# Optimization experiments

Hardware: AMD Instinct MI355X
Metric: run time of the kernel (lower is better)

## Reference

```python
import jax, jax.numpy as jnp
import numpy as np

N = 100000   # nodes
E = 1600000  # edges
IN, HID, OUT = 128, 128, 64

def setup_inputs() -> dict:
    key = jax.random.key(0)
    ks = jax.random.split(key, 18)
    def lin(k, i, o):
        kw, kb = jax.random.split(k)
        s = 1.0 / np.sqrt(i)
        return (jax.random.uniform(kw, (i, o), jnp.float32, -s, s),
                jax.random.uniform(kb, (o,), jnp.float32, -s, s))
    x = jax.random.normal(ks[0], (N, IN), jnp.float32)
    edge_index = jax.random.randint(ks[1], (2, E), 0, N, jnp.int64)
    W1, b1   = lin(ks[2], IN, HID)
    W21, b21 = lin(ks[3], IN, HID)
    W22, b22 = lin(ks[4], HID, HID)
    W31, b31 = lin(ks[5], IN, HID)
    W32, b32 = lin(ks[6], HID, HID)
    W33, b33 = lin(ks[7], HID, HID)
    Wa, ba   = lin(ks[8], HID, 1)
    Wf, bf   = lin(ks[9], HID, OUT)
    return dict(x=x, edge_index=edge_index, W1=W1, b1=b1, W21=W21, b21=b21,
                W22=W22, b22=b22, W31=W31, b31=b31, W32=W32, b32=b32,
                W33=W33, b33=b33, Wa=Wa, ba=ba, Wf=Wf, bf=bf)

def _gcn(x, W, b, src, dst, dinv):
    # PyG GCNConv: D^{-1/2}(A+I)D^{-1/2} X W + b, self-loops added.
    h = x @ W                                    # [N, F]
    norm = dinv[src] * dinv[dst]                 # [E]
    agg = jax.ops.segment_sum(h[src] * norm[:, None], dst, num_segments=N)
    agg = agg + h * (dinv * dinv)[:, None]       # self-loop contribution
    return agg + b

def reference(x, edge_index, W1, b1, W21, b21, W22, b22, W31, b31,
              W32, b32, W33, b33, Wa, ba, Wf, bf):
    src, dst = edge_index[0], edge_index[1]
    # degree with self-loops (in-degree at target nodes)
    deg = jax.ops.segment_sum(jnp.ones(E, x.dtype), dst, num_segments=N) + 1.0
    dinv = jax.lax.rsqrt(deg)
    h1 = jax.nn.relu(_gcn(x, W1, b1, src, dst, dinv))
    h2 = jax.nn.relu(_gcn(x, W21, b21, src, dst, dinv))
    h2 = jax.nn.relu(_gcn(h2, W22, b22, src, dst, dinv))
    h3 = jax.nn.relu(_gcn(x, W31, b31, src, dst, dinv))
    h3 = jax.nn.relu(_gcn(h3, W32, b32, src, dst, dinv))
    h3 = jax.nn.relu(_gcn(h3, W33, b33, src, dst, dinv))
    H = jnp.stack([h1, h2, h3], axis=1)          # [N, 3, HID]
    scores = H @ Wa + ba                         # [N, 3, 1]
    w = jax.nn.softmax(scores, axis=1)
    h_meta = jnp.sum(w * H, axis=1)              # [N, HID]
    h_out = h_meta + h1
    return h_out @ Wf + bf                       # [N, OUT]
```

## Files before the change

### kernel.cpp

```cpp
#include <hip/hip_runtime.h>
#include <hip/hip_bf16.h>

#define HIDF 128
#define OUTF 64
#define SCAN_B 256
#define BK_SHIFT 7

typedef __attribute__((ext_vector_type(8))) short bf16x8;
typedef __attribute__((ext_vector_type(4))) float f32x4;

__device__ __forceinline__ float us2f(unsigned u_lo16) {
    return __uint_as_float(u_lo16 << 16);
}
__device__ __forceinline__ unsigned short f2us(float f) {
    __hip_bfloat16 h = __float2bfloat16(f);
    return *reinterpret_cast<unsigned short*>(&h);
}
__device__ __forceinline__ unsigned pack2(float a, float b) {
    return (unsigned)f2us(a) | ((unsigned)f2us(b) << 16);
}

__global__ __launch_bounds__(256) void deg_zero(int* __restrict__ d, int N) {
    int i = blockIdx.x * 256 + threadIdx.x;
    if (i < N) d[i] = 0;
}

__global__ __launch_bounds__(256) void deg_count(const int* __restrict__ ei, int* __restrict__ d, int E) {
    int e = blockIdx.x * 256 + threadIdx.x;
    if (e < E) atomicAdd(&d[ei[E + e]], 1);
}

__global__ __launch_bounds__(256) void scanA(const int* __restrict__ degi, int* __restrict__ blocksum, int N) {
    __shared__ int red[256];
    const int b = blockIdx.x;
    const int chunk = (N + SCAN_B - 1) / SCAN_B;
    const int lo = b * chunk, hi = min(lo + chunk, N);
    int s = 0;
    for (int i = lo + threadIdx.x; i < hi; i += 256) s += degi[i];
    red[threadIdx.x] = s;
    __syncthreads();
    for (int off = 128; off; off >>= 1) {
        if (threadIdx.x < off) red[threadIdx.x] += red[threadIdx.x + off];
        __syncthreads();
    }
    if (threadIdx.x == 0) blocksum[b] = red[0];
}

__global__ __launch_bounds__(256) void scanB(const int* __restrict__ blocksum, int* __restrict__ blockoff) {
    __shared__ int ps[256];
    const int t = threadIdx.x;
    ps[t] = blocksum[t];
    __syncthreads();
    for (int off = 1; off < 256; off <<= 1) {
        int v = ps[t];
        int u = (t >= off) ? ps[t - off] : 0;
        __syncthreads();
        ps[t] = v + u;
        __syncthreads();
    }
    blockoff[t] = (t == 0) ? 0 : ps[t - 1];
}

__global__ __launch_bounds__(256) void scanC(const int* __restrict__ degi,
                                             const int* __restrict__ blockoff,
                                             int* __restrict__ cursor,
                                             float* __restrict__ dinv, int N) {
    __shared__ int ps[256];
    const int b = blockIdx.x;
    const int chunk = (N + SCAN_B - 1) / SCAN_B;
    const int lo = b * chunk, hi = min(lo + chunk, N);
    const int tchunk = (chunk + 255) / 256;
    const int tlo = lo + threadIdx.x * tchunk;
    const int thi = min(tlo + tchunk, hi);
    int s = 0;
    for (int i = tlo; i < thi; ++i) s += degi[i];
    ps[threadIdx.x] = s;
    __syncthreads();
    for (int off = 1; off < 256; off <<= 1) {
        int v = ps[threadIdx.x];
        int u = (threadIdx.x >= off) ? ps[threadIdx.x - off] : 0;
        __syncthreads();
        ps[threadIdx.x] = v + u;
        __syncthreads();
    }
    int base = blockoff[b] + ((threadIdx.x == 0) ? 0 : ps[threadIdx.x - 1]);
    for (int i = tlo; i < thi; ++i) {
        int d = degi[i];
        cursor[i] = base;
        base += d;
        dinv[i] = rsqrtf((float)d + 1.f);
    }
}

__global__ __launch_bounds__(256) void bcur_init(const int* __restrict__ cursor,
                                                 int* __restrict__ bcur, int N, int NBK) {
    int b = blockIdx.x * 256 + threadIdx.x;
    if (b < NBK) bcur[b * 64] = cursor[b << BK_SHIFT];
}

__global__ __launch_bounds__(256) void bucket_scatter(const int* __restrict__ ei,
                                                      int* __restrict__ bcur,
                                                      int2* __restrict__ edg, int E) {
    int e = blockIdx.x * 256 + threadIdx.x;
    if (e >= E) return;
    int src = ei[e];
    int dst = ei[E + e];
    int pos = atomicAdd(&bcur[(dst >> BK_SHIFT) * 64], 1);
    edg[pos] = make_int2(src, dst);
}

__global__ __launch_bounds__(256) void final_scatter(const int2* __restrict__ edg,
                                                     int* __restrict__ cursor,
                                                     int* __restrict__ csr_src, int E) {
    int p = blockIdx.x * 256 + threadIdx.x;
    if (p >= E) return;
    int2 sd = edg[p];
    int pos = atomicAdd(&cursor[sd.y], 1);
    csr_src[pos] = sd.x;
}

__global__ __launch_bounds__(256) void cvt_scale(const float* __restrict__ X,
                                                 const float* __restrict__ dinv,
                                                 unsigned short* __restrict__ TB, int N) {
    int g = blockIdx.x * 256 + threadIdx.x;
    if (g >= N * 32) return;
    int n = g >> 5;
    float dv = dinv[n];
    float4 v = ((const float4*)X)[g];
    ushort4 o;
    o.x = f2us(v.x * dv); o.y = f2us(v.y * dv);
    o.z = f2us(v.z * dv); o.w = f2us(v.w * dv);
    ((ushort4*)TB)[g] = o;
}

__global__ __launch_bounds__(256) void cvt_w(const float* __restrict__ Wa0,
                                             const float* __restrict__ Wa1,
                                             const float* __restrict__ Wa2,
                                             const float* __restrict__ Wa3,
                                             const float* __restrict__ Wa4,
                                             const float* __restrict__ Wa5,
                                             unsigned short* __restrict__ WTB) {
    int t = blockIdx.x * 256 + threadIdx.x;
    if (t >= 6 * 16384) return;
    int m = t >> 14, local = t & 16383;
    int n = local >> 7, k = local & 127;
    const float* src = (m == 0) ? Wa0 : (m == 1) ? Wa1 : (m == 2) ? Wa2
                     : (m == 3) ? Wa3 : (m == 4) ? Wa4 : Wa5;
    WTB[t] = f2us(src[k * 128 + n]);
}

template <bool OUT_BF16>
__global__ __launch_bounds__(256) void agg_b(const unsigned short* __restrict__ TB,
                                             const float* __restrict__ dinv,
                                             const int* __restrict__ csr_src,
                                             const int* __restrict__ rend,
                                             void* __restrict__ O, int N) {
    const int n = (blockIdx.x * 256 + threadIdx.x) >> 6;
    const int lane = threadIdx.x & 63;
    if (n >= N) return;
    const int start = (n == 0) ? 0 : rend[n - 1];
    const int end   = rend[n];
    const unsigned* Tv = (const unsigned*)TB;

    float ax0 = 0.f, ay0 = 0.f, ax1 = 0.f, ay1 = 0.f;
    int e = start;
    for (; e + 8 <= end; e += 8) {
        int s0 = csr_src[e + 0], s1 = csr_src[e + 1], s2 = csr_src[e + 2], s3 = csr_src[e + 3];
        int s4 = csr_src[e + 4], s5 = csr_src[e + 5], s6 = csr_src[e + 6], s7 = csr_src[e + 7];
        unsigned v0 = Tv[(size_t)s0 * 64 + lane];
        unsigned v1 = Tv[(size_t)s1 * 64 + lane];
        unsigned v2 = Tv[(size_t)s2 * 64 + lane];
        unsigned v3 = Tv[(size_t)s3 * 64 + lane];
        unsigned v4 = Tv[(size_t)s4 * 64 + lane];
        unsigned v5 = Tv[(size_t)s5 * 64 + lane];
        unsigned v6 = Tv[(size_t)s6 * 64 + lane];
        unsigned v7 = Tv[(size_t)s7 * 64 + lane];
        ax0 += us2f(v0 & 0xffffu); ay0 += __uint_as_float(v0 & 0xffff0000u);
        ax1 += us2f(v1 & 0xffffu); ay1 += __uint_as_float(v1 & 0xffff0000u);
        ax0 += us2f(v2 & 0xffffu); ay0 += __uint_as_float(v2 & 0xffff0000u);
        ax1 += us2f(v3 & 0xffffu); ay1 += __uint_as_float(v3 & 0xffff0000u);
        ax0 += us2f(v4 & 0xffffu); ay0 += __uint_as_float(v4 & 0xffff0000u);
        ax1 += us2f(v5 & 0xffffu); ay1 += __uint_as_float(v5 & 0xffff0000u);
        ax0 += us2f(v6 & 0xffffu); ay0 += __uint_as_float(v6 & 0xffff0000u);
        ax1 += us2f(v7 & 0xffffu); ay1 += __uint_as_float(v7 & 0xffff0000u);
    }
    if (e + 4 <= end) {
        int s0 = csr_src[e + 0], s1 = csr_src[e + 1], s2 = csr_src[e + 2], s3 = csr_src[e + 3];
        unsigned v0 = Tv[(size_t)s0 * 64 + lane];
        unsigned v1 = Tv[(size_t)s1 * 64 + lane];
        unsigned v2 = Tv[(size_t)s2 * 64 + lane];
        unsigned v3 = Tv[(size_t)s3 * 64 + lane];
        ax0 += us2f(v0 & 0xffffu); ay0 += __uint_as_float(v0 & 0xffff0000u);
        ax1 += us2f(v1 & 0xffffu); ay1 += __uint_as_float(v1 & 0xffff0000u);
        ax0 += us2f(v2 & 0xffffu); ay0 += __uint_as_float(v2 & 0xffff0000u);
        ax1 += us2f(v3 & 0xffffu); ay1 += __uint_as_float(v3 & 0xffff0000u);
        e += 4;
    }
    for (; e < end; ++e) {
        int s = csr_src[e];
        unsigned v = Tv[(size_t)s * 64 + lane];
        ax0 += us2f(v & 0xffffu);
        ay0 += __uint_as_float(v & 0xffff0000u);
    }
    unsigned sv = Tv[(size_t)n * 64 + lane];
    ax0 += us2f(sv & 0xffffu);
    ay0 += __uint_as_float(sv & 0xffff0000u);
    const float dv = dinv[n];
    float ox = (ax0 + ax1) * dv;
    float oy = (ay0 + ay1) * dv;
    if (OUT_BF16) {
        ((unsigned*)O)[(size_t)n * 64 + lane] = pack2(ox, oy);
    } else {
        float2 o; o.x = ox; o.y = oy;
        ((float2*)O)[(size_t)n * 64 + lane] = o;
    }
}

__global__ __launch_bounds__(256) void agg_dual(const unsigned short* __restrict__ TB23,
                                                const float* __restrict__ dinv,
                                                const int* __restrict__ csr_src,
                                                const int* __restrict__ rend,
                                                unsigned* __restrict__ OA,
                                                unsigned* __restrict__ OB, int N) {
    const int n = (blockIdx.x * 256 + threadIdx.x) >> 6;
    const int lane = threadIdx.x & 63;
    if (n >= N) return;
    const int start = (n == 0) ? 0 : rend[n - 1];
    const int end   = rend[n];
    const unsigned* Tv = (const unsigned*)TB23;

    float ax2 = 0.f, ay2 = 0.f, bx2 = 0.f, by2 = 0.f;
    float ax3 = 0.f, ay3 = 0.f, bx3 = 0.f, by3 = 0.f;
    int e = start;
    for (; e + 4 <= end; e += 4) {
        int s0 = csr_src[e + 0], s1 = csr_src[e + 1], s2 = csr_src[e + 2], s3 = csr_src[e + 3];
        unsigned a0 = Tv[(size_t)s0 * 128 + lane];
        unsigned c0 = Tv[(size_t)s0 * 128 + 64 + lane];
        unsigned a1 = Tv[(size_t)s1 * 128 + lane];
        unsigned c1 = Tv[(size_t)s1 * 128 + 64 + lane];
        unsigned a2 = Tv[(size_t)s2 * 128 + lane];
        unsigned c2 = Tv[(size_t)s2 * 128 + 64 + lane];
        unsigned a3 = Tv[(size_t)s3 * 128 + lane];
        unsigned c3 = Tv[(size_t)s3 * 128 + 64 + lane];
        ax2 += us2f(a0 & 0xffffu); ay2 += __uint_as_float(a0 & 0xffff0000u);
        ax3 += us2f(c0 & 0xffffu); ay3 += __uint_as_float(c0 & 0xffff0000u);
        bx2 += us2f(a1 & 0xffffu); by2 += __uint_as_float(a1 & 0xffff0000u);
        bx3 += us2f(c1 & 0xffffu); by3 += __uint_as_float(c1 & 0xffff0000u);
        ax2 += us2f(a2 & 0xffffu); ay2 += __uint_as_float(a2 & 0xffff0000u);
        ax3 += us2f(c2 & 0xffffu); ay3 += __uint_as_float(c2 & 0xffff0000u);
        bx2 += us2f(a3 & 0xffffu); by2 += __uint_as_float(a3 & 0xffff0000u);
        bx3 += us2f(c3 & 0xffffu); by3 += __uint_as_float(c3 & 0xffff0000u);
    }
    for (; e < end; ++e) {
        int s = csr_src[e];
        unsigned a = Tv[(size_t)s * 128 + lane];
        unsigned c = Tv[(size_t)s * 128 + 64 + lane];
        ax2 += us2f(a & 0xffffu); ay2 += __uint_as_float(a & 0xffff0000u);
        ax3 += us2f(c & 0xffffu); ay3 += __uint_as_float(c & 0xffff0000u);
    }
    {
        unsigned a = Tv[(size_t)n * 128 + lane];
        unsigned c = Tv[(size_t)n * 128 + 64 + lane];
        ax2 += us2f(a & 0xffffu); ay2 += __uint_as_float(a & 0xffff0000u);
        ax3 += us2f(c & 0xffffu); ay3 += __uint_as_float(c & 0xffff0000u);
    }
    const float dv = dinv[n];
    OA[(size_t)n * 64 + lane] = pack2((ax2 + bx2) * dv, (ay2 + by2) * dv);
    OB[(size_t)n * 64 + lane] = pack2((ax3 + bx3) * dv, (ay3 + by3) * dv);
}

#define OM_F32 0
#define OM_BF16 1
#define OM_BF16_SR 2
template <int OMODE, int OSTRIDE>
__global__ __launch_bounds__(256) void gemm_mfma(const unsigned short* __restrict__ Xb,
                                                 const unsigned short* __restrict__ WT,
                                                 const float* __restrict__ bias,
                                                 const float* __restrict__ dinv,
                                                 void* __restrict__ T, int N) {
    __shared__ unsigned short Xs[64 * 128];
    __shared__ unsigned short Ws[128 * 128];
    const int tid = threadIdx.x;
    const int nb = blockIdx.x * 64;

    for (int c = tid; c < 2048; c += 256) {
        int n = c >> 4, kc = c & 15;
        ((uint4*)Ws)[(n << 4) | (kc ^ (n & 7))] = ((const uint4*)WT)[c];
    }
    for (int c = tid; c < 1024; c += 256) {
        int nl = c >> 4, kc = c & 15;
        int n = nb + nl;
        uint4 v = make_uint4(0u, 0u, 0u, 0u);
        if (n < N) v = ((const uint4*)(Xb + (size_t)n * HIDF))[kc];
        ((uint4*)Xs)[(nl << 4) | (kc ^ (nl & 7))] = v;
    }
    __syncthreads();

    const int wv   = tid >> 6;
    const int l    = tid & 63;
    const int row  = l & 15;
    const int kgrp = l >> 4;

    bf16x8 afr[4];
    #pragma unroll
    for (int kk = 0; kk < 4; ++kk) {
        int nl = 16 * wv + row;
        int kc = kk * 4 + kgrp;
        afr[kk] = *(const bf16x8*)(Xs + nl * 128 + ((kc ^ (nl & 7)) << 3));
    }

    f32x4 acc[8];
    #pragma unroll
    for (int nt = 0; nt < 8; ++nt) {
        float b = bias[nt * 16 + row];
        acc[nt] = (f32x4){b, b, b, b};
    }

    #pragma unroll
    for (int nt = 0; nt < 8; ++nt) {
        int col = nt * 16 + row;
        #pragma unroll
        for (int kk = 0; kk < 4; ++kk) {
            int kc = kk * 4 + kgrp;
            bf16x8 bfr = *(const bf16x8*)(Ws + col * 128 + ((kc ^ (col & 7)) << 3));
            acc[nt] = __builtin_amdgcn_mfma_f32_16x16x32_bf16(afr[kk], bfr, acc[nt], 0, 0, 0);
        }
    }

    float dv[4];
    if (OMODE == OM_BF16_SR) {
        #pragma unroll
        for (int r = 0; r < 4; ++r) {
            int grow = nb + 16 * wv + kgrp * 4 + r;
            dv[r] = (grow < N) ? dinv[grow] : 0.f;
        }
    }
    #pragma unroll
    for (int nt = 0; nt < 8; ++nt) {
        int gcol = nt * 16 + row;
        #pragma unroll
        for (int r = 0; r < 4; ++r) {
            int grow = nb + 16 * wv + kgrp * 4 + r;
            if (grow < N) {
                float v = acc[nt][r];
                if (OMODE == OM_BF16_SR) v = fmaxf(v, 0.f) * dv[r];
                if (OMODE == OM_F32) {
                    ((float*)T)[(size_t)grow * OSTRIDE + gcol] = v;
                } else {
                    ((unsigned short*)T)[(size_t)grow * OSTRIDE + gcol] = f2us(v);
                }
            }
        }
    }
}

__global__ __launch_bounds__(256) void meta_kernel(const float* __restrict__ H1,
                                                   const unsigned short* __restrict__ H2B,
                                                   const unsigned short* __restrict__ H3B,
                                                   const float* __restrict__ Wa,
                                                   const float* __restrict__ ba,
                                                   const float* __restrict__ Wf,
                                                   const float* __restrict__ bfb,
                                                   float* __restrict__ out, int N) {
    __shared__ float WfS[HIDF * OUTF];
    __shared__ float WaS[HIDF];
    __shared__ float hm[4][HIDF];
    const int tid = threadIdx.x;
    for (int i = tid; i < HIDF * OUTF; i += 256) WfS[i] = Wf[i];
    if (tid < HIDF) WaS[tid] = Wa[tid];
    __syncthreads();
    const float bav = ba[0];
    const int w = tid >> 6;
    const int l = tid & 63;
    const float bfv = bfb[l];
    const int iters = (N + 3) >> 2;

    for (int it = blockIdx.x; it < iters; it += gridDim.x) {
        const int n = it * 4 + w;
        __syncthreads();
        if (n < N) {
            const float* h1 = H1 + (size_t)n * HIDF;
            const unsigned short* h2 = H2B + (size_t)n * HIDF;
            const unsigned short* h3 = H3B + (size_t)n * HIDF;
            float h1a = fmaxf(h1[l], 0.f),       h1b = fmaxf(h1[l + 64], 0.f);
            float h2a = fmaxf(us2f(h2[l]), 0.f), h2b = fmaxf(us2f(h2[l + 64]), 0.f);
            float h3a = fmaxf(us2f(h3[l]), 0.f), h3b = fmaxf(us2f(h3[l + 64]), 0.f);
            float s1 = h1a * WaS[l] + h1b * WaS[l + 64];
            float s2 = h2a * WaS[l] + h2b * WaS[l + 64];
            float s3 = h3a * WaS[l] + h3b * WaS[l + 64];
            #pragma unroll
            for (int off = 32; off; off >>= 1) {
                s1 += __shfl_xor(s1, off);
                s2 += __shfl_xor(s2, off);
                s3 += __shfl_xor(s3, off);
            }
            s1 += bav; s2 += bav; s3 += bav;
            float m  = fmaxf(s1, fmaxf(s2, s3));
            float e1 = expf(s1 - m), e2 = expf(s2 - m), e3 = expf(s3 - m);
            float inv = 1.f / (e1 + e2 + e3);
            float w1 = e1 * inv, w2 = e2 * inv, w3 = e3 * inv;
            hm[w][l]      = w1 * h1a + w2 * h2a + w3 * h3a + h1a;
            hm[w][l + 64] = w1 * h1b + w2 * h2b + w3 * h3b + h1b;
        }
        __syncthreads();
        if (n < N) {
            float acc = bfv;
            #pragma unroll
            for (int k = 0; k < HIDF; ++k) acc = fmaf(hm[w][k], WfS[k * OUTF + l], acc);
            out[(size_t)n * OUTF + l] = acc;
        }
    }
}

extern "C" void kernel_launch(void* const* d_in, const int* in_sizes, int n_in,
                              void* d_out, int out_size, void* d_ws, size_t ws_size,
                              hipStream_t stream) {
    const float* x   = (const float*)d_in[0];
    const int*   ei  = (const int*)d_in[1];
    const float *W1  = (const float*)d_in[2],  *b1  = (const float*)d_in[3];
    const float *W21 = (const float*)d_in[4],  *b21 = (const float*)d_in[5];
    const float *W22 = (const float*)d_in[6],  *b22 = (const float*)d_in[7];
    const float *W31 = (const float*)d_in[8],  *b31 = (const float*)d_in[9];
    const float *W32 = (const float*)d_in[10], *b32 = (const float*)d_in[11];
    const float *W33 = (const float*)d_in[12], *b33 = (const float*)d_in[13];
    const float *Wa  = (const float*)d_in[14], *ba  = (const float*)d_in[15];
    const float *Wf  = (const float*)d_in[16], *bfb = (const float*)d_in[17];

    const int N = in_sizes[0] / HIDF;
    const int E = in_sizes[1] / 2;
    const int NBK = (N + 127) >> BK_SHIFT;

    int*   DEGI    = (int*)d_ws;
    int*   CURSOR  = DEGI + N;
    int*   CSR_SRC = CURSOR + N;
    int2*  EDG     = (int2*)(CSR_SRC + E);
    int*   BCUR    = (int*)(EDG + E);
    int*   BSUM    = BCUR + 1024 * 64;
    int*   BOFF    = BSUM + 256;
    float* DINV    = (float*)(BOFF + 256);
    unsigned short* TB23 = (unsigned short*)(DINV + N);
    unsigned* PXB  = (unsigned*)(TB23 + (size_t)N * 256);
    unsigned* AGA  = PXB + (size_t)N * 64;
    unsigned* AGB  = AGA + (size_t)N * 64;
    unsigned* H2B  = AGB + (size_t)N * 64;
    unsigned short* WTB = (unsigned short*)(H2B + (size_t)N * 64);

    const int gN    = (N + 255) / 256;
    const int gE    = (E + 255) / 256;
    const int gCVT  = (N * 32 + 255) / 256;
    const int gAGG  = (N * 64 + 255) / 256;
    const int gGEMM = (N + 63) / 64;
    const int gMETA = 2048;

    deg_zero<<<gN, 256, 0, stream>>>(DEGI, N);
    deg_count<<<gE, 256, 0, stream>>>(ei, DEGI, E);
    scanA<<<SCAN_B, 256, 0, stream>>>(DEGI, BSUM, N);
    scanB<<<1, 256, 0, stream>>>(BSUM, BOFF);
    scanC<<<SCAN_B, 256, 0, stream>>>(DEGI, BOFF, CURSOR, DINV, N);
    bcur_init<<<(NBK + 255) / 256, 256, 0, stream>>>(CURSOR, BCUR, N, NBK);
    bucket_scatter<<<gE, 256, 0, stream>>>(ei, BCUR, EDG, E);
    final_scatter<<<gE, 256, 0, stream>>>(EDG, CURSOR, CSR_SRC, E);
    cvt_w<<<384, 256, 0, stream>>>(W21, W31, W22, W32, W33, W1, WTB);

    unsigned short* TBX = TB23;

    cvt_scale<<<gCVT, 256, 0, stream>>>(x, DINV, TBX, N);
    agg_b<true><<<gAGG, 256, 0, stream>>>(TBX, DINV, CSR_SRC, CURSOR, PXB, N);

    gemm_mfma<OM_BF16_SR, 256><<<gGEMM, 256, 0, stream>>>((unsigned short*)PXB, WTB,         b21, DINV, TB23,       N);
    gemm_mfma<OM_BF16_SR, 256><<<gGEMM, 256, 0, stream>>>((unsigned short*)PXB, WTB + 16384, b31, DINV, TB23 + 128, N);
    agg_dual<<<gAGG, 256, 0, stream>>>(TB23, DINV, CSR_SRC, CURSOR, AGA, AGB, N);

    gemm_mfma<OM_BF16, 128><<<gGEMM, 256, 0, stream>>>((unsigned short*)AGA, WTB + 2 * 16384, b22, DINV, H2B, N);
    gemm_mfma<OM_BF16_SR, 128><<<gGEMM, 256, 0, stream>>>((unsigned short*)AGB, WTB + 3 * 16384, b32, DINV, TBX, N);
    agg_b<true><<<gAGG, 256, 0, stream>>>(TBX, DINV, CSR_SRC, CURSOR, AGA, N);
    gemm_mfma<OM_BF16, 128><<<gGEMM, 256, 0, stream>>>((unsigned short*)AGA, WTB + 4 * 16384, b33, DINV, AGB, N);

    float* H1F = (float*)TB23;
    gemm_mfma<OM_F32, 128><<<gGEMM, 256, 0, stream>>>((unsigned short*)PXB, WTB + 5 * 16384, b1, DINV, H1F, N);

    meta_kernel<<<gMETA, 256, 0, stream>>>(H1F, (const unsigned short*)H2B,
                                           (const unsigned short*)AGB, Wa, ba, Wf, bfb,
                                           (float*)d_out, N);
}
```

Baseline: 726.6 us.

## Pack bucketed edges, per-bucket final scatter, wider gathers in aggregation kernels

Bucketed edges are now packed into one 32-bit word (source shifted, with the low destination bits), halving the intermediate edge buffer. The final scatter runs one block per 128-node bucket instead of one thread per edge. The aggregation kernels gather 8-byte uint2 chunks: a wave covers two edges at once with half-waves, reduced by a shuffle, and the dual kernel reads both feature sets per lane contiguously. The meta kernel reads packed pairs. Edge packing assumes source ids fit in 25 bits, and the wider loads change the summation order.

```diff
diff --git a/kernel.cpp b/kernel.cpp
--- a/kernel.cpp
+++ b/kernel.cpp
@@ -11,6 +11,9 @@
 
 __device__ __forceinline__ float us2f(unsigned u_lo16) {
     return __uint_as_float(u_lo16 << 16);
+}
+__device__ __forceinline__ float hi2f(unsigned u) {
+    return __uint_as_float(u & 0xffff0000u);
 }
 __device__ __forceinline__ unsigned short f2us(float f) {
     __hip_bfloat16 h = __float2bfloat16(f);
@@ -100,23 +103,33 @@
 
 __global__ __launch_bounds__(256) void bucket_scatter(const int* __restrict__ ei,
                                                       int* __restrict__ bcur,
-                                                      int2* __restrict__ edg, int E) {
+                                                      unsigned* __restrict__ edg, int E) {
     int e = blockIdx.x * 256 + threadIdx.x;
     if (e >= E) return;
     int src = ei[e];
     int dst = ei[E + e];
     int pos = atomicAdd(&bcur[(dst >> BK_SHIFT) * 64], 1);
-    edg[pos] = make_int2(src, dst);
-}
-
-__global__ __launch_bounds__(256) void final_scatter(const int2* __restrict__ edg,
-                                                     int* __restrict__ cursor,
-                                                     int* __restrict__ csr_src, int E) {
-    int p = blockIdx.x * 256 + threadIdx.x;
-    if (p >= E) return;
-    int2 sd = edg[p];
-    int pos = atomicAdd(&cursor[sd.y], 1);
-    csr_src[pos] = sd.x;
+    edg[pos] = ((unsigned)src << BK_SHIFT) | (unsigned)(dst & ((1 << BK_SHIFT) - 1));
+}
+
+__global__ __launch_bounds__(256) void final_scatter_b(const unsigned* __restrict__ edg,
+                                                       const int* __restrict__ bcur,
+                                                       int* __restrict__ cursor,
+                                                       int* __restrict__ csr_src) {
+    const int b = blockIdx.x;
+    __shared__ int sstart;
+    if (threadIdx.x == 0) sstart = cursor[b << BK_SHIFT];
+    __syncthreads();
+    const int bstart = sstart;
+    const int bend   = bcur[b * 64];
+    const int base   = b << BK_SHIFT;
+    for (int p = bstart + threadIdx.x; p < bend; p += 256) {
+        unsigned u = edg[p];
+        int src = (int)(u >> BK_SHIFT);
+        int dst = base | (int)(u & ((1u << BK_SHIFT) - 1));
+        int pos = atomicAdd(&cursor[dst], 1);
+        csr_src[pos] = src;
+    }
 }
 
 __global__ __launch_bounds__(256) void cvt_scale(const float* __restrict__ X,
@@ -149,124 +162,102 @@
     WTB[t] = f2us(src[k * 128 + n]);
 }
 
-template <bool OUT_BF16>
-__global__ __launch_bounds__(256) void agg_b(const unsigned short* __restrict__ TB,
-                                             const float* __restrict__ dinv,
-                                             const int* __restrict__ csr_src,
-                                             const int* __restrict__ rend,
-                                             void* __restrict__ O, int N) {
+__global__ __launch_bounds__(256) void agg_b2(const unsigned short* __restrict__ TB,
+                                              const float* __restrict__ dinv,
+                                              const int* __restrict__ csr_src,
+                                              const int* __restrict__ rend,
+                                              unsigned* __restrict__ O, int N) {
     const int n = (blockIdx.x * 256 + threadIdx.x) >> 6;
-    const int lane = threadIdx.x & 63;
+    const int l = threadIdx.x & 63;
+    if (n >= N) return;
+    const int half = l >> 5;
+    const int sl   = l & 31;
+    const int start = (n == 0) ? 0 : rend[n - 1];
+    const int end   = rend[n];
+    const uint2* Tv = (const uint2*)TB;
+
+    float a0 = 0.f, a1 = 0.f, a2 = 0.f, a3 = 0.f;
+    int e = start;
+    for (; e + 8 <= end; e += 8) {
+        int sA = csr_src[e + 0 + half];
+        int sB = csr_src[e + 2 + half];
+        int sC = csr_src[e + 4 + half];
+        int sD = csr_src[e + 6 + half];
+        uint2 vA = Tv[(size_t)sA * 32 + sl];
+        uint2 vB = Tv[(size_t)sB * 32 + sl];
+        uint2 vC = Tv[(size_t)sC * 32 + sl];
+        uint2 vD = Tv[(size_t)sD * 32 + sl];
+        a0 += us2f(vA.x & 0xffffu); a1 += hi2f(vA.x); a2 += us2f(vA.y & 0xffffu); a3 += hi2f(vA.y);
+        a0 += us2f(vB.x & 0xffffu); a1 += hi2f(vB.x); a2 += us2f(vB.y & 0xffffu); a3 += hi2f(vB.y);
+        a0 += us2f(vC.x & 0xffffu); a1 += hi2f(vC.x); a2 += us2f(vC.y & 0xffffu); a3 += hi2f(vC.y);
+        a0 += us2f(vD.x & 0xffffu); a1 += hi2f(vD.x); a2 += us2f(vD.y & 0xffffu); a3 += hi2f(vD.y);
+    }
+    for (; e + 2 <= end; e += 2) {
+        int s = csr_src[e + half];
+        uint2 v = Tv[(size_t)s * 32 + sl];
+        a0 += us2f(v.x & 0xffffu); a1 += hi2f(v.x); a2 += us2f(v.y & 0xffffu); a3 += hi2f(v.y);
+    }
+    if (e < end && half == 0) {
+        int s = csr_src[e];
+        uint2 v = Tv[(size_t)s * 32 + sl];
+        a0 += us2f(v.x & 0xffffu); a1 += hi2f(v.x); a2 += us2f(v.y & 0xffffu); a3 += hi2f(v.y);
+    }
+    if (half == 0) {
+        uint2 v = Tv[(size_t)n * 32 + sl];
+        a0 += us2f(v.x & 0xffffu); a1 += hi2f(v.x); a2 += us2f(v.y & 0xffffu); a3 += hi2f(v.y);
+    }
+    a0 += __shfl_xor(a0, 32); a1 += __shfl_xor(a1, 32);
+    a2 += __shfl_xor(a2, 32); a3 += __shfl_xor(a3, 32);
+    if (half == 0) {
+        const float dv = dinv[n];
+        uint2 o;
+        o.x = pack2(a0 * dv, a1 * dv);
+        o.y = pack2(a2 * dv, a3 * dv);
+        ((uint2*)O)[(size_t)n * 32 + sl] = o;
+    }
+}
+
+__global__ __launch_bounds__(256) void agg_dual2(const unsigned short* __restrict__ TB23,
+                                                 const float* __restrict__ dinv,
+                                                 const int* __restrict__ csr_src,
+                                                 const int* __restrict__ rend,
+                                                 unsigned* __restrict__ OA,
+                                                 unsigned* __restrict__ OB, int N) {
+    const int n = (blockIdx.x * 256 + threadIdx.x) >> 6;
+    const int l = threadIdx.x & 63;
     if (n >= N) return;
     const int start = (n == 0) ? 0 : rend[n - 1];
     const int end   = rend[n];
-    const unsigned* Tv = (const unsigned*)TB;
-
-    float ax0 = 0.f, ay0 = 0.f, ax1 = 0.f, ay1 = 0.f;
-    int e = start;
-    for (; e + 8 <= end; e += 8) {
-        int s0 = csr_src[e + 0], s1 = csr_src[e + 1], s2 = csr_src[e + 2], s3 = csr_src[e + 3];
-        int s4 = csr_src[e + 4], s5 = csr_src[e + 5], s6 = csr_src[e + 6], s7 = csr_src[e + 7];
-        unsigned v0 = Tv[(size_t)s0 * 64 + lane];
-        unsigned v1 = Tv[(size_t)s1 * 64 + lane];
-        unsigned v2 = Tv[(size_t)s2 * 64 + lane];
-        unsigned v3 = Tv[(size_t)s3 * 64 + lane];
-        unsigned v4 = Tv[(size_t)s4 * 64 + lane];
-        unsigned v5 = Tv[(size_t)s5 * 64 + lane];
-        unsigned v6 = Tv[(size_t)s6 * 64 + lane];
-        unsigned v7 = Tv[(size_t)s7 * 64 + lane];
-        ax0 += us2f(v0 & 0xffffu); ay0 += __uint_as_float(v0 & 0xffff0000u);
-        ax1 += us2f(v1 & 0xffffu); ay1 += __uint_as_float(v1 & 0xffff0000u);
-        ax0 += us2f(v2 & 0xffffu); ay0 += __uint_as_float(v2 & 0xffff0000u);
-        ax1 += us2f(v3 & 0xffffu); ay1 += __uint_as_float(v3 & 0xffff0000u);
-        ax0 += us2f(v4 & 0xffffu); ay0 += __uint_as_float(v4 & 0xffff0000u);
-        ax1 += us2f(v5 & 0xffffu); ay1 += __uint_as_float(v5 & 0xffff0000u);
-        ax0 += us2f(v6 & 0xffffu); ay0 += __uint_as_float(v6 & 0xffff0000u);
-        ax1 += us2f(v7 & 0xffffu); ay1 += __uint_as_float(v7 & 0xffff0000u);
-    }
-    if (e + 4 <= end) {
-        int s0 = csr_src[e + 0], s1 = csr_src[e + 1], s2 = csr_src[e + 2], s3 = csr_src[e + 3];
-        unsigned v0 = Tv[(size_t)s0 * 64 + lane];
-        unsigned v1 = Tv[(size_t)s1 * 64 + lane];
-        unsigned v2 = Tv[(size_t)s2 * 64 + lane];
-        unsigned v3 = Tv[(size_t)s3 * 64 + lane];
-        ax0 += us2f(v0 & 0xffffu); ay0 += __uint_as_float(v0 & 0xffff0000u);
-        ax1 += us2f(v1 & 0xffffu); ay1 += __uint_as_float(v1 & 0xffff0000u);
-        ax0 += us2f(v2 & 0xffffu); ay0 += __uint_as_float(v2 & 0xffff0000u);
-        ax1 += us2f(v3 & 0xffffu); ay1 += __uint_as_float(v3 & 0xffff0000u);
-        e += 4;
-    }
-    for (; e < end; ++e) {
-        int s = csr_src[e];
-        unsigned v = Tv[(size_t)s * 64 + lane];
-        ax0 += us2f(v & 0xffffu);
-        ay0 += __uint_as_float(v & 0xffff0000u);
-    }
-    unsigned sv = Tv[(size_t)n * 64 + lane];
-    ax0 += us2f(sv & 0xffffu);
-    ay0 += __uint_as_float(sv & 0xffff0000u);
-    const float dv = dinv[n];
-    float ox = (ax0 + ax1) * dv;
-    float oy = (ay0 + ay1) * dv;
-    if (OUT_BF16) {
-        ((unsigned*)O)[(size_t)n * 64 + lane] = pack2(ox, oy);
-    } else {
-        float2 o; o.x = ox; o.y = oy;
-        ((float2*)O)[(size_t)n * 64 + lane] = o;
-    }
-}
-
-__global__ __launch_bounds__(256) void agg_dual(const unsigned short* __restrict__ TB23,
-                                                const float* __restrict__ dinv,
-                                                const int* __restrict__ csr_src,
-                                                const int* __restrict__ rend,
-                                                unsigned* __restrict__ OA,
-                                                unsigned* __restrict__ OB, int N) {
-    const int n = (blockIdx.x * 256 + threadIdx.x) >> 6;
-    const int lane = threadIdx.x & 63;
-    if (n >= N) return;
-    const int start = (n == 0) ? 0 : rend[n - 1];
-    const int end   = rend[n];
-    const unsigned* Tv = (const unsigned*)TB23;
-
-    float ax2 = 0.f, ay2 = 0.f, bx2 = 0.f, by2 = 0.f;
-    float ax3 = 0.f, ay3 = 0.f, bx3 = 0.f, by3 = 0.f;
+    const uint2* Tv = (const uint2*)TB23;
+
+    float a0 = 0.f, a1 = 0.f, a2 = 0.f, a3 = 0.f;
     int e = start;
     for (; e + 4 <= end; e += 4) {
         int s0 = csr_src[e + 0], s1 = csr_src[e + 1], s2 = csr_src[e + 2], s3 = csr_src[e + 3];
-        unsigned a0 = Tv[(size_t)s0 * 128 + lane];
-        unsigned c0 = Tv[(size_t)s0 * 128 + 64 + lane];
-        unsigned a1 = Tv[(size_t)s1 * 128 + lane];
-        unsigned c1 = Tv[(size_t)s1 * 128 + 64 + lane];
-        unsigned a2 = Tv[(size_t)s2 * 128 + lane];
-        unsigned c2 = Tv[(size_t)s2 * 128 + 64 + lane];
-        unsigned a3 = Tv[(size_t)s3 * 128 + lane];
-        unsigned c3 = Tv[(size_t)s3 * 128 + 64 + lane];
-        ax2 += us2f(a0 & 0xffffu); ay2 += __uint_as_float(a0 & 0xffff0000u);
-        ax3 += us2f(c0 & 0xffffu); ay3 += __uint_as_float(c0 & 0xffff0000u);
-        bx2 += us2f(a1 & 0xffffu); by2 += __uint_as_float(a1 & 0xffff0000u);
-        bx3 += us2f(c1 & 0xffffu); by3 += __uint_as_float(c1 & 0xffff0000u);
-        ax2 += us2f(a2 & 0xffffu); ay2 += __uint_as_float(a2 & 0xffff0000u);
-        ax3 += us2f(c2 & 0xffffu); ay3 += __uint_as_float(c2 & 0xffff0000u);
-        bx2 += us2f(a3 & 0xffffu); by2 += __uint_as_float(a3 & 0xffff0000u);
-        bx3 += us2f(c3 & 0xffffu); by3 += __uint_as_float(c3 & 0xffff0000u);
+        uint2 v0 = Tv[(size_t)s0 * 64 + l];
+        uint2 v1 = Tv[(size_t)s1 * 64 + l];
+        uint2 v2 = Tv[(size_t)s2 * 64 + l];
+        uint2 v3 = Tv[(size_t)s3 * 64 + l];
+        a0 += us2f(v0.x & 0xffffu); a1 += hi2f(v0.x); a2 += us2f(v0.y & 0xffffu); a3 += hi2f(v0.y);
+        a0 += us2f(v1.x & 0xffffu); a1 += hi2f(v1.x); a2 += us2f(v1.y & 0xffffu); a3 += hi2f(v1.y);
+        a0 += us2f(v2.x & 0xffffu); a1 += hi2f(v2.x); a2 += us2f(v2.y & 0xffffu); a3 += hi2f(v2.y);
+        a0 += us2f(v3.x & 0xffffu); a1 += hi2f(v3.x); a2 += us2f(v3.y & 0xffffu); a3 += hi2f(v3.y);
     }
     for (; e < end; ++e) {
         int s = csr_src[e];
-        unsigned a = Tv[(size_t)s * 128 + lane];
-        unsigned c = Tv[(size_t)s * 128 + 64 + lane];
-        ax2 += us2f(a & 0xffffu); ay2 += __uint_as_float(a & 0xffff0000u);
-        ax3 += us2f(c & 0xffffu); ay3 += __uint_as_float(c & 0xffff0000u);
+        uint2 v = Tv[(size_t)s * 64 + l];
+        a0 += us2f(v.x & 0xffffu); a1 += hi2f(v.x); a2 += us2f(v.y & 0xffffu); a3 += hi2f(v.y);
     }
     {
-        unsigned a = Tv[(size_t)n * 128 + lane];
-        unsigned c = Tv[(size_t)n * 128 + 64 + lane];
-        ax2 += us2f(a & 0xffffu); ay2 += __uint_as_float(a & 0xffff0000u);
-        ax3 += us2f(c & 0xffffu); ay3 += __uint_as_float(c & 0xffff0000u);
+        uint2 v = Tv[(size_t)n * 64 + l];
+        a0 += us2f(v.x & 0xffffu); a1 += hi2f(v.x); a2 += us2f(v.y & 0xffffu); a3 += hi2f(v.y);
     }
     const float dv = dinv[n];
-    OA[(size_t)n * 64 + lane] = pack2((ax2 + bx2) * dv, (ay2 + by2) * dv);
-    OB[(size_t)n * 64 + lane] = pack2((ax3 + bx3) * dv, (ay3 + by3) * dv);
+    uint2 o;
+    o.x = pack2(a0 * dv, a1 * dv);
+    o.y = pack2(a2 * dv, a3 * dv);
+    if (l < 32) ((uint2*)OA)[(size_t)n * 32 + l] = o;
+    else        ((uint2*)OB)[(size_t)n * 32 + (l - 32)] = o;
 }
 
 #define OM_F32 0
@@ -355,8 +346,8 @@
 }
 
 __global__ __launch_bounds__(256) void meta_kernel(const float* __restrict__ H1,
-                                                   const unsigned short* __restrict__ H2B,
-                                                   const unsigned short* __restrict__ H3B,
+                                                   const unsigned* __restrict__ H2B,
+                                                   const unsigned* __restrict__ H3B,
                                                    const float* __restrict__ Wa,
                                                    const float* __restrict__ ba,
                                                    const float* __restrict__ Wf,
@@ -379,15 +370,16 @@
         const int n = it * 4 + w;
         __syncthreads();
         if (n < N) {
-            const float* h1 = H1 + (size_t)n * HIDF;
-            const unsigned short* h2 = H2B + (size_t)n * HIDF;
-            const unsigned short* h3 = H3B + (size_t)n * HIDF;
-            float h1a = fmaxf(h1[l], 0.f),       h1b = fmaxf(h1[l + 64], 0.f);
-            float h2a = fmaxf(us2f(h2[l]), 0.f), h2b = fmaxf(us2f(h2[l + 64]), 0.f);
-            float h3a = fmaxf(us2f(h3[l]), 0.f), h3b = fmaxf(us2f(h3[l + 64]), 0.f);
-            float s1 = h1a * WaS[l] + h1b * WaS[l + 64];
-            float s2 = h2a * WaS[l] + h2b * WaS[l + 64];
-            float s3 = h3a * WaS[l] + h3b * WaS[l + 64];
+            float2   p1 = ((const float2*)(H1 + (size_t)n * HIDF))[l];
+            unsigned u2 = H2B[(size_t)n * 64 + l];
+            unsigned u3 = H3B[(size_t)n * 64 + l];
+            float h1a = fmaxf(p1.x, 0.f),              h1b = fmaxf(p1.y, 0.f);
+            float h2a = fmaxf(us2f(u2 & 0xffffu), 0.f), h2b = fmaxf(hi2f(u2), 0.f);
+            float h3a = fmaxf(us2f(u3 & 0xffffu), 0.f), h3b = fmaxf(hi2f(u3), 0.f);
+            float wa0 = WaS[2 * l], wa1 = WaS[2 * l + 1];
+            float s1 = h1a * wa0 + h1b * wa1;
+            float s2 = h2a * wa0 + h2b * wa1;
+            float s3 = h3a * wa0 + h3b * wa1;
             #pragma unroll
             for (int off = 32; off; off >>= 1) {
                 s1 += __shfl_xor(s1, off);
@@ -399,8 +391,8 @@
             float e1 = expf(s1 - m), e2 = expf(s2 - m), e3 = expf(s3 - m);
             float inv = 1.f / (e1 + e2 + e3);
             float w1 = e1 * inv, w2 = e2 * inv, w3 = e3 * inv;
-            hm[w][l]      = w1 * h1a + w2 * h2a + w3 * h3a + h1a;
-            hm[w][l + 64] = w1 * h1b + w2 * h2b + w3 * h3b + h1b;
+            hm[w][2 * l]     = w1 * h1a + w2 * h2a + w3 * h3a + h1a;
+            hm[w][2 * l + 1] = w1 * h1b + w2 * h2b + w3 * h3b + h1b;
         }
         __syncthreads();
         if (n < N) {
@@ -430,14 +422,14 @@
     const int E = in_sizes[1] / 2;
     const int NBK = (N + 127) >> BK_SHIFT;
 
-    int*   DEGI    = (int*)d_ws;
-    int*   CURSOR  = DEGI + N;
-    int*   CSR_SRC = CURSOR + N;
-    int2*  EDG     = (int2*)(CSR_SRC + E);
-    int*   BCUR    = (int*)(EDG + E);
-    int*   BSUM    = BCUR + 1024 * 64;
-    int*   BOFF    = BSUM + 256;
-    float* DINV    = (float*)(BOFF + 256);
+    int*      DEGI    = (int*)d_ws;
+    int*      CURSOR  = DEGI + N;
+    int*      CSR_SRC = CURSOR + N;
+    unsigned* EDG     = (unsigned*)(CSR_SRC + E);
+    int*      BCUR    = (int*)(EDG + E);
+    int*      BSUM    = BCUR + 1024 * 64;
+    int*      BOFF    = BSUM + 256;
+    float*    DINV    = (float*)(BOFF + 256);
     unsigned short* TB23 = (unsigned short*)(DINV + N);
     unsigned* PXB  = (unsigned*)(TB23 + (size_t)N * 256);
     unsigned* AGA  = PXB + (size_t)N * 64;
@@ -459,27 +451,26 @@
     scanC<<<SCAN_B, 256, 0, stream>>>(DEGI, BOFF, CURSOR, DINV, N);
     bcur_init<<<(NBK + 255) / 256, 256, 0, stream>>>(CURSOR, BCUR, N, NBK);
     bucket_scatter<<<gE, 256, 0, stream>>>(ei, BCUR, EDG, E);
-    final_scatter<<<gE, 256, 0, stream>>>(EDG, CURSOR, CSR_SRC, E);
+    final_scatter_b<<<NBK, 256, 0, stream>>>(EDG, BCUR, CURSOR, CSR_SRC);
     cvt_w<<<384, 256, 0, stream>>>(W21, W31, W22, W32, W33, W1, WTB);
 
     unsigned short* TBX = TB23;
 
     cvt_scale<<<gCVT, 256, 0, stream>>>(x, DINV, TBX, N);
-    agg_b<true><<<gAGG, 256, 0, stream>>>(TBX, DINV, CSR_SRC, CURSOR, PXB, N);
+    agg_b2<<<gAGG, 256, 0, stream>>>(TBX, DINV, CSR_SRC, CURSOR, PXB, N);
 
     gemm_mfma<OM_BF16_SR, 256><<<gGEMM, 256, 0, stream>>>((unsigned short*)PXB, WTB,         b21, DINV, TB23,       N);
     gemm_mfma<OM_BF16_SR, 256><<<gGEMM, 256, 0, stream>>>((unsigned short*)PXB, WTB + 16384, b31, DINV, TB23 + 128, N);
-    agg_dual<<<gAGG, 256, 0, stream>>>(TB23, DINV, CSR_SRC, CURSOR, AGA, AGB, N);
+    agg_dual2<<<gAGG, 256, 0, stream>>>(TB23, DINV, CSR_SRC, CURSOR, AGA, AGB, N);
 
     gemm_mfma<OM_BF16, 128><<<gGEMM, 256, 0, stream>>>((unsigned short*)AGA, WTB + 2 * 16384, b22, DINV, H2B, N);
     gemm_mfma<OM_BF16_SR, 128><<<gGEMM, 256, 0, stream>>>((unsigned short*)AGB, WTB + 3 * 16384, b32, DINV, TBX, N);
-    agg_b<true><<<gAGG, 256, 0, stream>>>(TBX, DINV, CSR_SRC, CURSOR, AGA, N);
+    agg_b2<<<gAGG, 256, 0, stream>>>(TBX, DINV, CSR_SRC, CURSOR, AGA, N);
     gemm_mfma<OM_BF16, 128><<<gGEMM, 256, 0, stream>>>((unsigned short*)AGA, WTB + 4 * 16384, b33, DINV, AGB, N);
 
     float* H1F = (float*)TB23;
     gemm_mfma<OM_F32, 128><<<gGEMM, 256, 0, stream>>>((unsigned short*)PXB, WTB + 5 * 16384, b1, DINV, H1F, N);
 
-    meta_kernel<<<gMETA, 256, 0, stream>>>(H1F, (const unsigned short*)H2B,
-                                           (const unsigned short*)AGB, Wa, ba, Wf, bfb,
+    meta_kernel<<<gMETA, 256, 0, stream>>>(H1F, H2B, AGB, Wa, ba, Wf, bfb,
                                            (float*)d_out, N);
 }
```

Result: faster. 705.8 us (-2.9%).
